# Optimization experiments

Hardware: AMD Instinct MI355X
Metric: run time of the kernel (lower is better)

Reference implementation:

```python
import jax, jax.numpy as jnp
import numpy as np

B, N, T, C, H, HH, ED, HOR, OC = 16, 307, 12, 2, 64, 64, 8, 12, 1


def setup_inputs() -> dict:
    key = jax.random.key(0)
    ks = jax.random.split(key, 23)
    r = lambda i, shape: jax.random.normal(ks[i], shape, dtype=jnp.float32) * 0.1
    return dict(
        coeff_a=r(0, (B, N, T - 1, C)), coeff_b=r(1, (B, N, T - 1, C)),
        coeff_c=r(2, (B, N, T - 1, C)), coeff_d=r(3, (B, N, T - 1, C)),
        times=jnp.arange(T, dtype=jnp.float32),
        h_W=r(4, (C, H)), h_b=r(5, (H,)),
        z_W=r(6, (C, H)), z_b=r(7, (H,)),
        f_W_in=r(8, (H, HH)), f_b_in=r(9, (HH,)),
        f_W_mid=r(10, (HH, HH)), f_b_mid=r(11, (HH,)),
        f_W_out=r(12, (HH, H * C)), f_b_out=r(13, (H * C,)),
        g_W_in=r(14, (H, HH)), g_b_in=r(15, (HH,)),
        g_E=r(16, (N, ED)), g_Wpool=r(17, (ED, 2, HH, HH)), g_bpool=r(18, (ED, HH)),
        g_W_out=r(19, (HH, H * H)), g_b_out=r(20, (H * H,)),
        conv_W=r(21, (HOR * OC, H)), conv_b=r(22, (HOR * OC,)),
    )


def _forward(coeff_a, coeff_b, coeff_c, coeff_d, times,
             h_W, h_b, z_W, z_b,
             f_W_in, f_b_in, f_W_mid, f_b_mid, f_W_out, f_b_out,
             g_W_in, g_b_in, g_E, g_Wpool, g_bpool, g_W_out, g_b_out,
             conv_W, conv_b):
    n_int = times.shape[0] - 1

    def spline_deriv(t):
        # natural cubic spline derivative: b + (two_c + three_d*frac)*frac on interval idx
        idx = jnp.clip(jnp.searchsorted(times, t, side='right') - 1, 0, n_int - 1)
        frac = t - times[idx]
        bb = jnp.take(coeff_b, idx, axis=2)
        cc = jnp.take(coeff_c, idx, axis=2)
        dd = jnp.take(coeff_d, idx, axis=2)
        return bb + (cc + dd * frac) * frac  # (B,N,C)

    def func_f(h):
        x = jax.nn.relu(h @ f_W_in + f_b_in)
        x = jax.nn.relu(x @ f_W_mid + f_b_mid)
        x = (x @ f_W_out + f_b_out).reshape(*x.shape[:-1], H, C)
        return jnp.tanh(x)  # (B,N,H,C)

    # adaptive adjacency (constant across time, depends only on node embeddings)
    A = jax.nn.softmax(jax.nn.relu(g_E @ g_E.T), axis=1)       # (N,N)
    supports = jnp.stack([jnp.eye(N, dtype=A.dtype), A])       # (K=2,N,N)
    agc_W = jnp.einsum('nd,dkio->nkio', g_E, g_Wpool)          # (N,K,HH,HH)
    agc_b = g_E @ g_bpool                                      # (N,HH)

    def func_g(z):
        x = jax.nn.relu(z @ g_W_in + g_b_in)                   # (B,N,HH)
        x_g = jnp.einsum('knm,bmc->bnkc', supports, x)         # (B,N,K,HH)
        x = jnp.einsum('bnki,nkio->bno', x_g, agc_W) + agc_b   # (B,N,HH)
        x = jax.nn.relu(x)
        x = (x @ g_W_out + g_b_out).reshape(*x.shape[:-1], H, H)
        return jnp.tanh(x)  # (B,N,H,H)

    def vf(t, h, z):
        dX = spline_deriv(t)                                   # (B,N,C)
        f_v = func_f(h)                                        # (B,N,H,C)
        g_v = func_g(z)                                        # (B,N,H,H)
        dh = jnp.einsum('bnhc,bnc->bnh', f_v, dX)
        fg = jnp.einsum('bnij,bnjc->bnic', g_v, f_v)           # (B,N,H,C)
        dz = jnp.einsum('bnhc,bnc->bnh', fg, dX)
        return dh, dz

    # initial states from spline value at times[0] (= coeff_a at interval 0, frac 0)
    x0 = coeff_a[:, :, 0, :]                                   # (B,N,C)
    h0 = x0 @ h_W + h_b
    z0 = x0 @ z_W + z_b

    def step(carry, ts):
        h, z = carry
        t0, t1 = ts
        dt = t1 - t0
        k1h, k1z = vf(t0, h, z)
        k2h, k2z = vf(t0 + dt / 2, h + dt / 2 * k1h, z + dt / 2 * k1z)
        k3h, k3z = vf(t0 + dt / 2, h + dt / 2 * k2h, z + dt / 2 * k2z)
        k4h, k4z = vf(t1, h + dt * k3h, z + dt * k3z)
        h = h + dt / 6 * (k1h + 2 * k2h + 2 * k3h + k4h)
        z = z + dt / 6 * (k1z + 2 * k2z + 2 * k3z + k4z)
        return (h, z), None

    (hT, zT), _ = jax.lax.scan(step, (h0, z0), (times[:-1], times[1:]))

    # end_conv: Conv2d(1, HOR*OC, kernel=(1,H)) over (B,1,N,H) == linear over H
    out = jnp.einsum('bnh,oh->bon', zT, conv_W) + conv_b[None, :, None]  # (B,HOR*OC,N)
    out = out.reshape(B, HOR, OC, N).transpose(0, 1, 3, 2)               # (B,HOR,N,OC)
    return out


def reference(coeff_a, coeff_b, coeff_c, coeff_d, times,
              h_W, h_b, z_W, z_b,
              f_W_in, f_b_in, f_W_mid, f_b_mid, f_W_out, f_b_out,
              g_W_in, g_b_in, g_E, g_Wpool, g_bpool, g_W_out, g_b_out,
              conv_W, conv_b):
    return _forward(coeff_a, coeff_b, coeff_c, coeff_d, times,
                    h_W, h_b, z_W, z_b,
                    f_W_in, f_b_in, f_W_mid, f_b_mid, f_W_out, f_b_out,
                    g_W_in, g_b_in, g_E, g_Wpool, g_bpool, g_W_out, g_b_out,
                    conv_W, conv_b)
```

## Files before the change

kernel.cpp:

```cpp
#include <hip/hip_runtime.h>

#define NB 16
#define NN 307
#define NI 11

typedef __attribute__((ext_vector_type(8))) short bf16x8;
typedef __attribute__((ext_vector_type(4))) float f32x4;

#define OFF_ABF    0u
#define OFF_AGCWT  51200u
#define OFF_AGCB   1308672u
#define OFF_WT     1329152u
#define OFF_H      1460224u
#define OFF_Z      1774592u
#define OFF_KZ     2088960u
#define OFF_ACCZ   2403328u
#define OFF_XBF    2717696u
#define OFF_XGBF   2881536u
#define OFF_XT     3045376u
#define OFF_KHALL  3209216u

#define STG_STRIDE 314368u

__device__ __forceinline__ float tanh_fast(float x){
    float e = __expf(2.0f * x);
    return 1.0f - 2.0f * __builtin_amdgcn_rcpf(e + 1.0f);
}
__device__ __forceinline__ unsigned short f2bf(float f){
    unsigned u = __builtin_bit_cast(unsigned, f);
    unsigned r = u + 0x7FFFu + ((u >> 16) & 1u);
    return (unsigned short)(r >> 16);
}


__global__ void kA(const float* __restrict__ gE, unsigned short* __restrict__ Abf){
    int n = blockIdx.x;
    int lane = threadIdx.x;
    if (n >= NN){
#pragma unroll
        for (int ii = 0; ii < 5; ii++) Abf[n*320 + lane + 64*ii] = 0;
        return;
    }
    float en[8];
#pragma unroll
    for (int d = 0; d < 8; d++) en[d] = gE[n*8 + d];
    float vals[5];
    float mx = -1e30f;
#pragma unroll
    for (int ii = 0; ii < 5; ii++){
        int m = lane + 64*ii;
        float v = -1e30f;
        if (m < NN){
            float a = 0.f;
#pragma unroll
            for (int d = 0; d < 8; d++) a += en[d] * gE[m*8 + d];
            v = fmaxf(a, 0.f);
        }
        vals[ii] = v;
        mx = fmaxf(mx, v);
    }
#pragma unroll
    for (int off = 32; off >= 1; off >>= 1) mx = fmaxf(mx, __shfl_xor(mx, off, 64));
    float s = 0.f;
#pragma unroll
    for (int ii = 0; ii < 5; ii++){
        int m = lane + 64*ii;
        if (m < NN){ vals[ii] = __expf(vals[ii] - mx); s += vals[ii]; }
    }
#pragma unroll
    for (int off = 32; off >= 1; off >>= 1) s += __shfl_xor(s, off, 64);
    float inv = 1.f / s;
#pragma unroll
    for (int ii = 0; ii < 5; ii++){
        int m = lane + 64*ii;
        unsigned short v = 0;
        if (m < NN) v = f2bf(vals[ii] * inv);
        Abf[n*320 + m] = v;
    }
}

__global__ __launch_bounds__(256) void kAgcWT(const float* __restrict__ gE,
                                              const float* __restrict__ gWpool,
                                              unsigned short* __restrict__ agcWt){
    __shared__ float t[128*65];
    int tid = threadIdx.x;
    int n = blockIdx.x;
    float ge[8];
#pragma unroll
    for (int d = 0; d < 8; d++) ge[d] = gE[n*8 + d];
    for (int it = 0; it < 32; it++){
        int e = it*256 + tid;
        int o = e & 63, i = (e >> 6) & 63, kk = e >> 12;
        float acc = 0.f;
#pragma unroll
        for (int d = 0; d < 8; d++) acc += ge[d] * gWpool[((size_t)(d*2 + kk)*64 + i)*64 + o];
        t[(kk*64 + i)*65 + o] = acc;
    }
    __syncthreads();
    for (int it = 0; it < 32; it++){
        int e = it*256 + tid;
        int k = e & 127, o = e >> 7;
        agcWt[((size_t)n*64 + o)*128 + k] = f2bf(t[k*65 + o]);
    }
}

__global__ void kAgcB(const float* __restrict__ gE, const float* __restrict__ gbpool,
                      float* __restrict__ agcb){
    int gid = blockIdx.x*256 + threadIdx.x;
    if (gid >= NN*64) return;
    int o = gid & 63;
    int n = gid >> 6;
    float acc = 0.f;
#pragma unroll
    for (int d = 0; d < 8; d++) acc += gE[n*8 + d] * gbpool[d*64 + o];
    agcb[gid] = acc;
}

__global__ __launch_bounds__(256) void kWt(const float* __restrict__ WgOut,
                                           unsigned short* __restrict__ Wt_sw){
    __shared__ float t[64*65];
    int tid = threadIdx.x;
    int c0 = blockIdx.x*64;
    for (int it = 0; it < 16; it++){
        int e = it*256 + tid;
        int k = e >> 6, c = e & 63;
        t[k*65 + c] = WgOut[(size_t)k*4096 + c0 + c];
    }
    __syncthreads();
    for (int it = 0; it < 16; it++){
        int e = it*256 + tid;
        int c = e >> 6, k = e & 63;
        int ks = ((((k >> 3) ^ (c & 7)) << 3) | (k & 7));
        Wt_sw[(size_t)(c0 + c)*64 + ks] = f2bf(t[k*65 + c]);
    }
}

__global__ void kZeroTail(unsigned short* __restrict__ xT){
    int gid = blockIdx.x*256 + threadIdx.x;
    int mo = gid & 15, c = (gid >> 4) & 63, b = gid >> 10;
    xT[((size_t)b*64 + c)*320 + 304 + mo] = 0;
}

__global__ void kInit(const float* __restrict__ ca,
                      const float* __restrict__ hW, const float* __restrict__ hb,
                      const float* __restrict__ zW, const float* __restrict__ zb,
                      float* __restrict__ h, float* __restrict__ z){
    int gid = blockIdx.x*256 + threadIdx.x;
    int t = gid & 63;
    int bn = gid >> 6;
    float x0 = ca[bn*NI*2 + 0];
    float x1 = ca[bn*NI*2 + 1];
    h[gid] = x0*hW[t] + x1*hW[64 + t] + hb[t];
    z[gid] = x0*zW[t] + x1*zW[64 + t] + zb[t];
}

__global__ __launch_bounds__(256) void KH(
    const float* __restrict__ h0, float* __restrict__ khAll,
    const float* __restrict__ Cb, const float* __restrict__ Cc, const float* __restrict__ Cd,
    const float* __restrict__ WfIn, const float* __restrict__ fbIn,
    const float* __restrict__ WfMid, const float* __restrict__ fbMid,
    const float* __restrict__ WfOut, const float* __restrict__ fbOut)
{
    __shared__ float4 bufA[4][16];
    __shared__ float4 bufB[4][16];
    int tid = threadIdx.x;
    int wv = tid >> 6;
    int lane = tid & 63;
    int bn = blockIdx.x*4 + wv;
    int base = bn*64 + lane;

    float hv = h0[base];
    float acch = 0.f, khprev = 0.f;

#pragma unroll 1
    for (int stage = 0; stage < 44; stage++){
        int step = stage >> 2, s = stage & 3;
        float acoef = (s == 0) ? 0.f : (s == 3 ? 1.f : 0.5f);
        int idx; float frac;
        if (s == 0)        { idx = step;     frac = 0.f;  }
        else if (s < 3)    { idx = step;     frac = 0.5f; }
        else if (step < 10){ idx = step + 1; frac = 0.f;  }
        else               { idx = 10;       frac = 1.f;  }

        float sih = hv + acoef * khprev;
        ((float*)&bufA[wv][0])[lane] = sih;

        float a0 = fbIn[lane], a1 = 0.f, a2 = 0.f, a3 = 0.f;
#pragma unroll
        for (int k4 = 0; k4 < 16; k4 += 2){
            float4 s4 = bufA[wv][k4];
            float4 s5 = bufA[wv][k4+1];
            int k = k4*4;
            a0 += s4.x*WfIn[(k+0)*64 + lane];
            a1 += s4.y*WfIn[(k+1)*64 + lane];
            a2 += s4.z*WfIn[(k+2)*64 + lane];
            a3 += s4.w*WfIn[(k+3)*64 + lane];
            a0 += s5.x*WfIn[(k+4)*64 + lane];
            a1 += s5.y*WfIn[(k+5)*64 + lane];
            a2 += s5.z*WfIn[(k+6)*64 + lane];
            a3 += s5.w*WfIn[(k+7)*64 + lane];
        }
        float u = fmaxf((a0 + a1) + (a2 + a3), 0.f);
        ((float*)&bufB[wv][0])[lane] = u;

        float c0_ = fbMid[lane], c1_ = 0.f, c2_ = 0.f, c3_ = 0.f;
#pragma unroll
        for (int k4 = 0; k4 < 16; k4 += 2){
            float4 s4 = bufB[wv][k4];
            float4 s5 = bufB[wv][k4+1];
            int k = k4*4;
            c0_ += s4.x*WfMid[(k+0)*64 + lane];
            c1_ += s4.y*WfMid[(k+1)*64 + lane];
            c2_ += s4.z*WfMid[(k+2)*64 + lane];
            c3_ += s4.w*WfMid[(k+3)*64 + lane];
            c0_ += s5.x*WfMid[(k+4)*64 + lane];
            c1_ += s5.y*WfMid[(k+5)*64 + lane];
            c2_ += s5.z*WfMid[(k+6)*64 + lane];
            c3_ += s5.w*WfMid[(k+7)*64 + lane];
        }
        float u2v = fmaxf((c0_ + c1_) + (c2_ + c3_), 0.f);
        ((float*)&bufA[wv][0])[lane] = u2v;

        float f0a = fbOut[lane*2 + 0], f0b = 0.f;
        float f1a = fbOut[lane*2 + 1], f1b = 0.f;
#pragma unroll
        for (int k4 = 0; k4 < 16; k4 += 2){
            float4 s4 = bufA[wv][k4];
            float4 s5 = bufA[wv][k4+1];
            int k = k4*4;
            f0a += s4.x*WfOut[(k+0)*128 + lane*2+0]; f1a += s4.x*WfOut[(k+0)*128 + lane*2+1];
            f0b += s4.y*WfOut[(k+1)*128 + lane*2+0]; f1b += s4.y*WfOut[(k+1)*128 + lane*2+1];
            f0a += s4.z*WfOut[(k+2)*128 + lane*2+0]; f1a += s4.z*WfOut[(k+2)*128 + lane*2+1];
            f0b += s4.w*WfOut[(k+3)*128 + lane*2+0]; f1b += s4.w*WfOut[(k+3)*128 + lane*2+1];
            f0a += s5.x*WfOut[(k+4)*128 + lane*2+0]; f1a += s5.x*WfOut[(k+4)*128 + lane*2+1];
            f0b += s5.y*WfOut[(k+5)*128 + lane*2+0]; f1b += s5.y*WfOut[(k+5)*128 + lane*2+1];
            f0a += s5.z*WfOut[(k+6)*128 + lane*2+0]; f1a += s5.z*WfOut[(k+6)*128 + lane*2+1];
            f0b += s5.w*WfOut[(k+7)*128 + lane*2+0]; f1b += s5.w*WfOut[(k+7)*128 + lane*2+1];
        }
        float f0 = tanh_fast(f0a + f0b);
        float f1 = tanh_fast(f1a + f1b);

        int cb = (bn*NI + idx)*2;
        float b0 = Cb[cb], b1 = Cb[cb+1];
        float c0 = Cc[cb], c1 = Cc[cb+1];
        float d0 = Cd[cb], d1 = Cd[cb+1];
        float dx0 = b0 + (c0 + d0*frac)*frac;
        float dx1 = b1 + (c1 + d1*frac)*frac;

        float khv = f0*dx0 + f1*dx1;
        khAll[(size_t)stage*STG_STRIDE + base] = khv;
        if (s == 0)      acch = khv;
        else if (s < 3)  acch += 2.f*khv;
        else             hv = hv + (1.f/6.f)*(acch + khv);
        khprev = khv;
    }
}

__global__ __launch_bounds__(256) void Kz1(
    const float* __restrict__ z, const float* __restrict__ kz,
    unsigned short* __restrict__ xbf, unsigned short* __restrict__ xT,
    const float* __restrict__ WgIn, const float* __restrict__ gbIn,
    int stage, float acoef)
{
    __shared__ float4 bufZ[4][16];
    int tid = threadIdx.x;
    int wv = tid >> 6;
    int lane = tid & 63;
    int bn = blockIdx.x*4 + wv;
    int base = bn*64 + lane;
    int b = (int)((unsigned)bn / 307u);
    int n = bn - b*307;

    float siz = z[base];
    if (stage > 0) siz += acoef * kz[base];
    ((float*)&bufZ[wv][0])[lane] = siz;

    float xa = gbIn[lane], xb = 0.f;
#pragma unroll
    for (int k4 = 0; k4 < 16; k4 += 2){
        float4 z4 = bufZ[wv][k4];
        float4 z5 = bufZ[wv][k4+1];
        int k = k4*4;
        xa += z4.x*WgIn[(k+0)*64 + lane];
        xb += z4.y*WgIn[(k+1)*64 + lane];
        xa += z4.z*WgIn[(k+2)*64 + lane];
        xb += z4.w*WgIn[(k+3)*64 + lane];
        xa += z5.x*WgIn[(k+4)*64 + lane];
        xb += z5.y*WgIn[(k+5)*64 + lane];
        xa += z5.z*WgIn[(k+6)*64 + lane];
        xb += z5.w*WgIn[(k+7)*64 + lane];
    }
    unsigned short xbfv = f2bf(fmaxf(xa + xb, 0.f));
    xbf[((size_t)n*16 + b)*64 + lane] = xbfv;
    xT[((size_t)b*64 + lane)*320 + n] = xbfv;
}

__global__ __launch_bounds__(256) void KXG(
    const unsigned short* __restrict__ xT, const unsigned short* __restrict__ Abf,
    unsigned short* __restrict__ xgbf)
{
    int tid = threadIdx.x, lane = tid & 63, wv = tid >> 6;
    int quad = lane >> 4, l15 = lane & 15;
    int b = blockIdx.x / 20, nt = blockIdx.x % 20;
    int n0 = nt*16;

    f32x4 acc = {0.f,0.f,0.f,0.f};
#pragma unroll
    for (int mt = 0; mt < 10; mt++){
        bf16x8 a  = *(const bf16x8*)(Abf + (size_t)(n0 + l15)*320 + mt*32 + quad*8);
        bf16x8 bb = *(const bf16x8*)(xT + ((size_t)b*64 + wv*16 + l15)*320 + mt*32 + quad*8);
        acc = __builtin_amdgcn_mfma_f32_16x16x32_bf16(a, bb, acc, 0, 0, 0);
    }
#pragma unroll
    for (int r = 0; r < 4; r++){
        int n = n0 + quad*4 + r;
        xgbf[((size_t)n*16 + b)*64 + wv*16 + l15] = f2bf(acc[r]);
    }
}

__global__ __launch_bounds__(256, 3) void K2f(
    float* __restrict__ z, const float* __restrict__ khS,
    float* __restrict__ kz, float* __restrict__ accz,
    const unsigned short* __restrict__ xbf, const unsigned short* __restrict__ xgbf,
    const unsigned short* __restrict__ agcWt, const float* __restrict__ agcb,
    const unsigned short* __restrict__ Wt_sw, const float* __restrict__ gbOut,
    int stage)
{
    __shared__ unsigned short WtL[256*64];
    __shared__ unsigned short Ybf[64*68];
    __shared__ float dzl[4*16*5];
    int tid = threadIdx.x, lane = tid & 63, wv = tid >> 6;
    int quad = lane >> 4, l15 = lane & 15;
    int nt = blockIdx.x >> 4, cg = blockIdx.x & 15;
    int n0 = nt*4;
    int nw = n0 + wv;
    int n = nw < NN ? nw : NN-1;
    int C0 = cg*256;

#pragma unroll
    for (int it = 0; it < 8; it++){
        int seg = it*256 + wv*64 + lane;
        const unsigned short* src = Wt_sw + (size_t)C0*64 + (size_t)seg*8;
        __builtin_amdgcn_global_load_lds(
            (const __attribute__((address_space(1))) void*)src,
            (__attribute__((address_space(3))) void*)(WtL + (it*256 + wv*64)*8),
            16, 0, 0);
    }

    float4 khr[4];
#pragma unroll
    for (int c = 0; c < 4; c++)
        khr[c] = *(const float4*)(khS + ((size_t)l15*NN + n)*64 + c*16 + quad*4);

    {
        const size_t xrow = ((size_t)n*16 + l15)*64;
        bf16x8 a[4];
        a[0] = *(const bf16x8*)(xbf  + xrow + 0  + quad*8);
        a[1] = *(const bf16x8*)(xbf  + xrow + 32 + quad*8);
        a[2] = *(const bf16x8*)(xgbf + xrow + 0  + quad*8);
        a[3] = *(const bf16x8*)(xgbf + xrow + 32 + quad*8);
#pragma unroll
        for (int ot = 0; ot < 4; ot++){
            f32x4 acc = {0.f,0.f,0.f,0.f};
#pragma unroll
            for (int kt = 0; kt < 4; kt++){
                bf16x8 bbb = *(const bf16x8*)(agcWt + ((size_t)n*64 + ot*16 + l15)*128 + kt*32 + quad*8);
                acc = __builtin_amdgcn_mfma_f32_16x16x32_bf16(a[kt], bbb, acc, 0, 0, 0);
            }
            float gb = agcb[n*64 + ot*16 + l15];
#pragma unroll
            for (int r = 0; r < 4; r++)
                Ybf[(wv*16 + quad*4 + r)*68 + ot*16 + l15] = f2bf(fmaxf(acc[r] + gb, 0.f));
        }
    }

    __syncthreads();

    bf16x8 bb0 = *(const bf16x8*)(Ybf + (wv*16 + l15)*68 + 0  + quad*8);
    bf16x8 bb1 = *(const bf16x8*)(Ybf + (wv*16 + l15)*68 + 32 + quad*8);

    int sw = l15 & 7;
#pragma unroll
    for (int i4 = 0; i4 < 4; i4++){
        float pacc = 0.f;
#pragma unroll
        for (int c4 = 0; c4 < 4; c4++){
            int ct = i4*4 + c4;
            int row = ct*16 + l15;
            f32x4 acc = {0.f,0.f,0.f,0.f};
            bf16x8 a0 = *(const bf16x8*)(WtL + row*64 + (((quad)     ^ sw) << 3));
            acc = __builtin_amdgcn_mfma_f32_16x16x32_bf16(a0, bb0, acc, 0, 0, 0);
            bf16x8 a1 = *(const bf16x8*)(WtL + row*64 + (((4 + quad) ^ sw) << 3));
            acc = __builtin_amdgcn_mfma_f32_16x16x32_bf16(a1, bb1, acc, 0, 0, 0);
            float4 gb4 = *(const float4*)(gbOut + C0 + ct*16 + quad*4);
            float4 kh4 = khr[c4];
            pacc += tanh_fast(acc[0] + gb4.x) * kh4.x
                  + tanh_fast(acc[1] + gb4.y) * kh4.y
                  + tanh_fast(acc[2] + gb4.z) * kh4.z
                  + tanh_fast(acc[3] + gb4.w) * kh4.w;
        }
        pacc += __shfl_xor(pacc, 16, 64);
        pacc += __shfl_xor(pacc, 32, 64);
        if (quad == 0) dzl[(wv*16 + l15)*5 + i4] = pacc;
    }

    {
        int w = tid >> 6, bb_ = (tid >> 2) & 15, il = tid & 3;
        int nn = n0 + w;
        if (nn < NN){
            size_t addr = ((size_t)bb_*NN + nn)*64 + cg*4 + il;
            float v = dzl[(w*16 + bb_)*5 + il];
            kz[addr] = v;
            if (stage == 0)      accz[addr] = v;
            else if (stage < 3)  accz[addr] += 2.f*v;
            else                 z[addr] += (1.f/6.f)*(accz[addr] + v);
        }
    }
}

__global__ __launch_bounds__(256) void kOut(const float* __restrict__ z,
                                            const float* __restrict__ convW,
                                            const float* __restrict__ convB,
                                            float* __restrict__ out){
    int gid = blockIdx.x*256 + threadIdx.x;
    if (gid >= NB*NN) return;
    int b = gid / NN, n = gid % NN;
    float zr[64];
    const float4* zp = (const float4*)(z + (size_t)gid*64);
#pragma unroll
    for (int k4 = 0; k4 < 16; k4++){
        float4 v = zp[k4];
        zr[k4*4+0] = v.x; zr[k4*4+1] = v.y; zr[k4*4+2] = v.z; zr[k4*4+3] = v.w;
    }
#pragma unroll
    for (int o = 0; o < 12; o++){
        float acc = convB[o];
#pragma unroll
        for (int hh = 0; hh < 64; hh++) acc += zr[hh]*convW[o*64 + hh];
        out[(b*12 + o)*NN + n] = acc;
    }
}

extern "C" void kernel_launch(void* const* d_in, const int* in_sizes, int n_in,
                              void* d_out, int out_size, void* d_ws, size_t ws_size,
                              hipStream_t stream)
{
    const float* coeff_a = (const float*)d_in[0];
    const float* coeff_b = (const float*)d_in[1];
    const float* coeff_c = (const float*)d_in[2];
    const float* coeff_d = (const float*)d_in[3];
    const float* hW     = (const float*)d_in[5];
    const float* hb     = (const float*)d_in[6];
    const float* zW     = (const float*)d_in[7];
    const float* zb     = (const float*)d_in[8];
    const float* WfIn   = (const float*)d_in[9];
    const float* fbIn   = (const float*)d_in[10];
    const float* WfMid  = (const float*)d_in[11];
    const float* fbMid  = (const float*)d_in[12];
    const float* WfOut  = (const float*)d_in[13];
    const float* fbOut  = (const float*)d_in[14];
    const float* WgIn   = (const float*)d_in[15];
    const float* gbIn   = (const float*)d_in[16];
    const float* gE     = (const float*)d_in[17];
    const float* gWpool = (const float*)d_in[18];
    const float* gbpool = (const float*)d_in[19];
    const float* WgOut  = (const float*)d_in[20];
    const float* gbOut  = (const float*)d_in[21];
    const float* convW  = (const float*)d_in[22];
    const float* convB  = (const float*)d_in[23];

    float* ws = (float*)d_ws;
    unsigned short* Abf   = (unsigned short*)(ws + OFF_ABF);
    unsigned short* agcWt = (unsigned short*)(ws + OFF_AGCWT);
    float*          agcb  = ws + OFF_AGCB;
    unsigned short* Wt_sw = (unsigned short*)(ws + OFF_WT);
    float* h     = ws + OFF_H;
    float* z     = ws + OFF_Z;
    float* kz    = ws + OFF_KZ;
    float* accz  = ws + OFF_ACCZ;
    unsigned short* xbf  = (unsigned short*)(ws + OFF_XBF);
    unsigned short* xgbf = (unsigned short*)(ws + OFF_XGBF);
    unsigned short* xT   = (unsigned short*)(ws + OFF_XT);
    float* khAll = ws + OFF_KHALL;
    float* out = (float*)d_out;

    kA        <<<320, 64,  0, stream>>>(gE, Abf);
    kAgcWT    <<<NN,  256, 0, stream>>>(gE, gWpool, agcWt);
    kAgcB     <<<77,  256, 0, stream>>>(gE, gbpool, agcb);
    kWt       <<<64,  256, 0, stream>>>(WgOut, Wt_sw);
    kZeroTail <<<64,  256, 0, stream>>>(xT);
    kInit     <<<1228,256, 0, stream>>>(coeff_a, hW, hb, zW, zb, h, z);

    KH<<<1228, 256, 0, stream>>>(h, khAll, coeff_b, coeff_c, coeff_d,
                                 WfIn, fbIn, WfMid, fbMid, WfOut, fbOut);

    const float acoef[4] = {0.f, 0.5f, 0.5f, 1.f};
    for (int step = 0; step < 11; step++){
        for (int s = 0; s < 4; s++){
            const float* khS = khAll + (size_t)(step*4 + s)*STG_STRIDE;
            Kz1<<<1228, 256, 0, stream>>>(z, kz, xbf, xT, WgIn, gbIn, s, acoef[s]);
            KXG<<<320, 256, 0, stream>>>(xT, Abf, xgbf);
            K2f<<<1232, 256, 0, stream>>>(z, khS, kz, accz, xbf, xgbf,
                                          agcWt, agcb, Wt_sw, gbOut, s);
        }
    }
    kOut<<<20, 256, 0, stream>>>(z, convW, convB, out);
}
```

Measured before the change: 2.094 ms.

## Fuse g input layer into graph aggregation kernel via MFMA; two nodes per wave in KH

Merges the per-stage Kz1 and KXG kernels into one KXZ kernel. It computes relu(z_stage @ WgIn + b) with bf16 MFMA into a shared-memory transposed tile, then runs the adjacency MFMA from LDS, which removes one launch per stage (44 in total) and the global xT round trip. The cost is that each of the 20 node-tile blocks per batch recomputes the full input projection for all 307 nodes, so that work is duplicated 20x. Separately, KH now processes two nodes per wave so each weight load is shared across two rows, halving its grid.

Result: slower. 3.243 ms (+54.9%).

```diff
diff --git a/kernel.cpp b/kernel.cpp
--- a/kernel.cpp
+++ b/kernel.cpp
@@ -5,6 +5,7 @@
 #define NI 11
 
 typedef __attribute__((ext_vector_type(8))) short bf16x8;
+typedef __attribute__((ext_vector_type(4))) short bf16x4;
 typedef __attribute__((ext_vector_type(4))) float f32x4;
 
 #define OFF_ABF    0u
@@ -17,7 +18,7 @@
 #define OFF_ACCZ   2403328u
 #define OFF_XBF    2717696u
 #define OFF_XGBF   2881536u
-#define OFF_XT     3045376u
+#define OFF_WGINT  3045376u
 #define OFF_KHALL  3209216u
 
 #define STG_STRIDE 314368u
@@ -135,10 +136,10 @@
     }
 }
 
-__global__ void kZeroTail(unsigned short* __restrict__ xT){
+__global__ void kWgInT(const float* __restrict__ WgIn, unsigned short* __restrict__ WgInT){
     int gid = blockIdx.x*256 + threadIdx.x;
-    int mo = gid & 15, c = (gid >> 4) & 63, b = gid >> 10;
-    xT[((size_t)b*64 + c)*320 + 304 + mo] = 0;
+    int c = gid >> 6, k = gid & 63;
+    WgInT[gid] = f2bf(WgIn[k*64 + c]);
 }
 
 __global__ void kInit(const float* __restrict__ ca,
@@ -161,16 +162,17 @@
     const float* __restrict__ WfMid, const float* __restrict__ fbMid,
     const float* __restrict__ WfOut, const float* __restrict__ fbOut)
 {
-    __shared__ float4 bufA[4][16];
-    __shared__ float4 bufB[4][16];
+    __shared__ float4 bufA[4][2][16];
+    __shared__ float4 bufB[4][2][16];
     int tid = threadIdx.x;
     int wv = tid >> 6;
     int lane = tid & 63;
-    int bn = blockIdx.x*4 + wv;
-    int base = bn*64 + lane;
-
-    float hv = h0[base];
-    float acch = 0.f, khprev = 0.f;
+    int bn0 = (blockIdx.x*4 + wv)*2;
+    int base0 = bn0*64 + lane;
+
+    float hv0 = h0[base0];
+    float hv1 = h0[base0 + 64];
+    float acch0 = 0.f, khp0 = 0.f, acch1 = 0.f, khp1 = 0.f;
 
 #pragma unroll 1
     for (int stage = 0; stage < 44; stage++){
@@ -182,139 +184,178 @@
         else if (step < 10){ idx = step + 1; frac = 0.f;  }
         else               { idx = 10;       frac = 1.f;  }
 
-        float sih = hv + acoef * khprev;
-        ((float*)&bufA[wv][0])[lane] = sih;
+        ((float*)&bufA[wv][0][0])[lane] = hv0 + acoef*khp0;
+        ((float*)&bufA[wv][1][0])[lane] = hv1 + acoef*khp1;
 
         float a0 = fbIn[lane], a1 = 0.f, a2 = 0.f, a3 = 0.f;
+        float e0 = fbIn[lane], e1 = 0.f, e2 = 0.f, e3 = 0.f;
 #pragma unroll
         for (int k4 = 0; k4 < 16; k4 += 2){
-            float4 s4 = bufA[wv][k4];
-            float4 s5 = bufA[wv][k4+1];
+            float4 s4 = bufA[wv][0][k4];
+            float4 s5 = bufA[wv][0][k4+1];
+            float4 t4 = bufA[wv][1][k4];
+            float4 t5 = bufA[wv][1][k4+1];
             int k = k4*4;
-            a0 += s4.x*WfIn[(k+0)*64 + lane];
-            a1 += s4.y*WfIn[(k+1)*64 + lane];
-            a2 += s4.z*WfIn[(k+2)*64 + lane];
-            a3 += s4.w*WfIn[(k+3)*64 + lane];
-            a0 += s5.x*WfIn[(k+4)*64 + lane];
-            a1 += s5.y*WfIn[(k+5)*64 + lane];
-            a2 += s5.z*WfIn[(k+6)*64 + lane];
-            a3 += s5.w*WfIn[(k+7)*64 + lane];
-        }
-        float u = fmaxf((a0 + a1) + (a2 + a3), 0.f);
-        ((float*)&bufB[wv][0])[lane] = u;
+            float w;
+            w = WfIn[(k+0)*64 + lane]; a0 += s4.x*w; e0 += t4.x*w;
+            w = WfIn[(k+1)*64 + lane]; a1 += s4.y*w; e1 += t4.y*w;
+            w = WfIn[(k+2)*64 + lane]; a2 += s4.z*w; e2 += t4.z*w;
+            w = WfIn[(k+3)*64 + lane]; a3 += s4.w*w; e3 += t4.w*w;
+            w = WfIn[(k+4)*64 + lane]; a0 += s5.x*w; e0 += t5.x*w;
+            w = WfIn[(k+5)*64 + lane]; a1 += s5.y*w; e1 += t5.y*w;
+            w = WfIn[(k+6)*64 + lane]; a2 += s5.z*w; e2 += t5.z*w;
+            w = WfIn[(k+7)*64 + lane]; a3 += s5.w*w; e3 += t5.w*w;
+        }
+        ((float*)&bufB[wv][0][0])[lane] = fmaxf((a0 + a1) + (a2 + a3), 0.f);
+        ((float*)&bufB[wv][1][0])[lane] = fmaxf((e0 + e1) + (e2 + e3), 0.f);
 
         float c0_ = fbMid[lane], c1_ = 0.f, c2_ = 0.f, c3_ = 0.f;
+        float g0_ = fbMid[lane], g1_ = 0.f, g2_ = 0.f, g3_ = 0.f;
 #pragma unroll
         for (int k4 = 0; k4 < 16; k4 += 2){
-            float4 s4 = bufB[wv][k4];
-            float4 s5 = bufB[wv][k4+1];
+            float4 s4 = bufB[wv][0][k4];
+            float4 s5 = bufB[wv][0][k4+1];
+            float4 t4 = bufB[wv][1][k4];
+            float4 t5 = bufB[wv][1][k4+1];
             int k = k4*4;
-            c0_ += s4.x*WfMid[(k+0)*64 + lane];
-            c1_ += s4.y*WfMid[(k+1)*64 + lane];
-            c2_ += s4.z*WfMid[(k+2)*64 + lane];
-            c3_ += s4.w*WfMid[(k+3)*64 + lane];
-            c0_ += s5.x*WfMid[(k+4)*64 + lane];
-            c1_ += s5.y*WfMid[(k+5)*64 + lane];
-            c2_ += s5.z*WfMid[(k+6)*64 + lane];
-            c3_ += s5.w*WfMid[(k+7)*64 + lane];
-        }
-        float u2v = fmaxf((c0_ + c1_) + (c2_ + c3_), 0.f);
-        ((float*)&bufA[wv][0])[lane] = u2v;
-
-        float f0a = fbOut[lane*2 + 0], f0b = 0.f;
-        float f1a = fbOut[lane*2 + 1], f1b = 0.f;
+            float w;
+            w = WfMid[(k+0)*64 + lane]; c0_ += s4.x*w; g0_ += t4.x*w;
+            w = WfMid[(k+1)*64 + lane]; c1_ += s4.y*w; g1_ += t4.y*w;
+            w = WfMid[(k+2)*64 + lane]; c2_ += s4.z*w; g2_ += t4.z*w;
+            w = WfMid[(k+3)*64 + lane]; c3_ += s4.w*w; g3_ += t4.w*w;
+            w = WfMid[(k+4)*64 + lane]; c0_ += s5.x*w; g0_ += t5.x*w;
+            w = WfMid[(k+5)*64 + lane]; c1_ += s5.y*w; g1_ += t5.y*w;
+            w = WfMid[(k+6)*64 + lane]; c2_ += s5.z*w; g2_ += t5.z*w;
+            w = WfMid[(k+7)*64 + lane]; c3_ += s5.w*w; g3_ += t5.w*w;
+        }
+        ((float*)&bufA[wv][0][0])[lane] = fmaxf((c0_ + c1_) + (c2_ + c3_), 0.f);
+        ((float*)&bufA[wv][1][0])[lane] = fmaxf((g0_ + g1_) + (g2_ + g3_), 0.f);
+
+        float p0a = fbOut[lane*2 + 0], p0b = 0.f;
+        float p1a = fbOut[lane*2 + 1], p1b = 0.f;
+        float q0a = fbOut[lane*2 + 0], q0b = 0.f;
+        float q1a = fbOut[lane*2 + 1], q1b = 0.f;
 #pragma unroll
         for (int k4 = 0; k4 < 16; k4 += 2){
-            float4 s4 = bufA[wv][k4];
-            float4 s5 = bufA[wv][k4+1];
+            float4 s4 = bufA[wv][0][k4];
+            float4 s5 = bufA[wv][0][k4+1];
+            float4 t4 = bufA[wv][1][k4];
+            float4 t5 = bufA[wv][1][k4+1];
             int k = k4*4;
-            f0a += s4.x*WfOut[(k+0)*128 + lane*2+0]; f1a += s4.x*WfOut[(k+0)*128 + lane*2+1];
-            f0b += s4.y*WfOut[(k+1)*128 + lane*2+0]; f1b += s4.y*WfOut[(k+1)*128 + lane*2+1];
-            f0a += s4.z*WfOut[(k+2)*128 + lane*2+0]; f1a += s4.z*WfOut[(k+2)*128 + lane*2+1];
-            f0b += s4.w*WfOut[(k+3)*128 + lane*2+0]; f1b += s4.w*WfOut[(k+3)*128 + lane*2+1];
-            f0a += s5.x*WfOut[(k+4)*128 + lane*2+0]; f1a += s5.x*WfOut[(k+4)*128 + lane*2+1];
-            f0b += s5.y*WfOut[(k+5)*128 + lane*2+0]; f1b += s5.y*WfOut[(k+5)*128 + lane*2+1];
-            f0a += s5.z*WfOut[(k+6)*128 + lane*2+0]; f1a += s5.z*WfOut[(k+6)*128 + lane*2+1];
-            f0b += s5.w*WfOut[(k+7)*128 + lane*2+0]; f1b += s5.w*WfOut[(k+7)*128 + lane*2+1];
-        }
-        float f0 = tanh_fast(f0a + f0b);
-        float f1 = tanh_fast(f1a + f1b);
-
-        int cb = (bn*NI + idx)*2;
-        float b0 = Cb[cb], b1 = Cb[cb+1];
-        float c0 = Cc[cb], c1 = Cc[cb+1];
-        float d0 = Cd[cb], d1 = Cd[cb+1];
-        float dx0 = b0 + (c0 + d0*frac)*frac;
-        float dx1 = b1 + (c1 + d1*frac)*frac;
-
-        float khv = f0*dx0 + f1*dx1;
-        khAll[(size_t)stage*STG_STRIDE + base] = khv;
-        if (s == 0)      acch = khv;
-        else if (s < 3)  acch += 2.f*khv;
-        else             hv = hv + (1.f/6.f)*(acch + khv);
-        khprev = khv;
-    }
-}
-
-__global__ __launch_bounds__(256) void Kz1(
+            float w0, w1;
+            w0 = WfOut[(k+0)*128 + lane*2+0]; w1 = WfOut[(k+0)*128 + lane*2+1];
+            p0a += s4.x*w0; p1a += s4.x*w1; q0a += t4.x*w0; q1a += t4.x*w1;
+            w0 = WfOut[(k+1)*128 + lane*2+0]; w1 = WfOut[(k+1)*128 + lane*2+1];
+            p0b += s4.y*w0; p1b += s4.y*w1; q0b += t4.y*w0; q1b += t4.y*w1;
+            w0 = WfOut[(k+2)*128 + lane*2+0]; w1 = WfOut[(k+2)*128 + lane*2+1];
+            p0a += s4.z*w0; p1a += s4.z*w1; q0a += t4.z*w0; q1a += t4.z*w1;
+            w0 = WfOut[(k+3)*128 + lane*2+0]; w1 = WfOut[(k+3)*128 + lane*2+1];
+            p0b += s4.w*w0; p1b += s4.w*w1; q0b += t4.w*w0; q1b += t4.w*w1;
+            w0 = WfOut[(k+4)*128 + lane*2+0]; w1 = WfOut[(k+4)*128 + lane*2+1];
+            p0a += s5.x*w0; p1a += s5.x*w1; q0a += t5.x*w0; q1a += t5.x*w1;
+            w0 = WfOut[(k+5)*128 + lane*2+0]; w1 = WfOut[(k+5)*128 + lane*2+1];
+            p0b += s5.y*w0; p1b += s5.y*w1; q0b += t5.y*w0; q1b += t5.y*w1;
+            w0 = WfOut[(k+6)*128 + lane*2+0]; w1 = WfOut[(k+6)*128 + lane*2+1];
+            p0a += s5.z*w0; p1a += s5.z*w1; q0a += t5.z*w0; q1a += t5.z*w1;
+            w0 = WfOut[(k+7)*128 + lane*2+0]; w1 = WfOut[(k+7)*128 + lane*2+1];
+            p0b += s5.w*w0; p1b += s5.w*w1; q0b += t5.w*w0; q1b += t5.w*w1;
+        }
+        float f00 = tanh_fast(p0a + p0b);
+        float f01 = tanh_fast(p1a + p1b);
+        float f10 = tanh_fast(q0a + q0b);
+        float f11 = tanh_fast(q1a + q1b);
+
+        int cb0 = (bn0*NI + idx)*2;
+        int cb1 = cb0 + NI*2;
+        float dx00 = Cb[cb0]   + (Cc[cb0]   + Cd[cb0]*frac)*frac;
+        float dx01 = Cb[cb0+1] + (Cc[cb0+1] + Cd[cb0+1]*frac)*frac;
+        float dx10 = Cb[cb1]   + (Cc[cb1]   + Cd[cb1]*frac)*frac;
+        float dx11 = Cb[cb1+1] + (Cc[cb1+1] + Cd[cb1+1]*frac)*frac;
+
+        float kh0 = f00*dx00 + f01*dx01;
+        float kh1 = f10*dx10 + f11*dx11;
+        khAll[(size_t)stage*STG_STRIDE + base0]      = kh0;
+        khAll[(size_t)stage*STG_STRIDE + base0 + 64] = kh1;
+        if (s == 0)     { acch0 = kh0;        acch1 = kh1; }
+        else if (s < 3) { acch0 += 2.f*kh0;   acch1 += 2.f*kh1; }
+        else            { hv0 += (1.f/6.f)*(acch0 + kh0); hv1 += (1.f/6.f)*(acch1 + kh1); }
+        khp0 = kh0; khp1 = kh1;
+    }
+}
+
+__global__ __launch_bounds__(256) void KXZ(
     const float* __restrict__ z, const float* __restrict__ kz,
-    unsigned short* __restrict__ xbf, unsigned short* __restrict__ xT,
-    const float* __restrict__ WgIn, const float* __restrict__ gbIn,
+    const unsigned short* __restrict__ WgInT, const float* __restrict__ gbIn,
+    const unsigned short* __restrict__ Abf,
+    unsigned short* __restrict__ xbf, unsigned short* __restrict__ xgbf,
     int stage, float acoef)
 {
-    __shared__ float4 bufZ[4][16];
-    int tid = threadIdx.x;
-    int wv = tid >> 6;
-    int lane = tid & 63;
-    int bn = blockIdx.x*4 + wv;
-    int base = bn*64 + lane;
-    int b = (int)((unsigned)bn / 307u);
-    int n = bn - b*307;
-
-    float siz = z[base];
-    if (stage > 0) siz += acoef * kz[base];
-    ((float*)&bufZ[wv][0])[lane] = siz;
-
-    float xa = gbIn[lane], xb = 0.f;
-#pragma unroll
-    for (int k4 = 0; k4 < 16; k4 += 2){
-        float4 z4 = bufZ[wv][k4];
-        float4 z5 = bufZ[wv][k4+1];
-        int k = k4*4;
-        xa += z4.x*WgIn[(k+0)*64 + lane];
-        xb += z4.y*WgIn[(k+1)*64 + lane];
-        xa += z4.z*WgIn[(k+2)*64 + lane];
-        xb += z4.w*WgIn[(k+3)*64 + lane];
-        xa += z5.x*WgIn[(k+4)*64 + lane];
-        xb += z5.y*WgIn[(k+5)*64 + lane];
-        xa += z5.z*WgIn[(k+6)*64 + lane];
-        xb += z5.w*WgIn[(k+7)*64 + lane];
-    }
-    unsigned short xbfv = f2bf(fmaxf(xa + xb, 0.f));
-    xbf[((size_t)n*16 + b)*64 + lane] = xbfv;
-    xT[((size_t)b*64 + lane)*320 + n] = xbfv;
-}
-
-__global__ __launch_bounds__(256) void KXG(
-    const unsigned short* __restrict__ xT, const unsigned short* __restrict__ Abf,
-    unsigned short* __restrict__ xgbf)
-{
+    __shared__ unsigned short xLT[64*328];
     int tid = threadIdx.x, lane = tid & 63, wv = tid >> 6;
     int quad = lane >> 4, l15 = lane & 15;
     int b = blockIdx.x / 20, nt = blockIdx.x % 20;
     int n0 = nt*16;
+    int cc = wv*16 + l15;
+
+    bf16x8 wb0 = *(const bf16x8*)(WgInT + cc*64 + quad*8);
+    bf16x8 wb1 = *(const bf16x8*)(WgInT + cc*64 + 32 + quad*8);
+    float gb = gbIn[cc];
+    bool writer = (nt == 0);
+
+#pragma unroll 1
+    for (int mt = 0; mt < 20; mt++){
+        int m = mt*16 + l15;
+        bf16x8 af0 = {0,0,0,0,0,0,0,0};
+        bf16x8 af1 = {0,0,0,0,0,0,0,0};
+        if (m < NN){
+            const float* zp = z + ((size_t)b*NN + m)*64;
+            float4 x0 = *(const float4*)(zp + quad*8);
+            float4 x1 = *(const float4*)(zp + quad*8 + 4);
+            float4 y0 = *(const float4*)(zp + 32 + quad*8);
+            float4 y1 = *(const float4*)(zp + 32 + quad*8 + 4);
+            if (stage > 0){
+                const float* kp = kz + ((size_t)b*NN + m)*64;
+                float4 k0 = *(const float4*)(kp + quad*8);
+                float4 k1 = *(const float4*)(kp + quad*8 + 4);
+                float4 k2 = *(const float4*)(kp + 32 + quad*8);
+                float4 k3 = *(const float4*)(kp + 32 + quad*8 + 4);
+                x0.x += acoef*k0.x; x0.y += acoef*k0.y; x0.z += acoef*k0.z; x0.w += acoef*k0.w;
+                x1.x += acoef*k1.x; x1.y += acoef*k1.y; x1.z += acoef*k1.z; x1.w += acoef*k1.w;
+                y0.x += acoef*k2.x; y0.y += acoef*k2.y; y0.z += acoef*k2.z; y0.w += acoef*k2.w;
+                y1.x += acoef*k3.x; y1.y += acoef*k3.y; y1.z += acoef*k3.z; y1.w += acoef*k3.w;
+            }
+            unsigned short* p0 = (unsigned short*)&af0;
+            unsigned short* p1 = (unsigned short*)&af1;
+            p0[0]=f2bf(x0.x); p0[1]=f2bf(x0.y); p0[2]=f2bf(x0.z); p0[3]=f2bf(x0.w);
+            p0[4]=f2bf(x1.x); p0[5]=f2bf(x1.y); p0[6]=f2bf(x1.z); p0[7]=f2bf(x1.w);
+            p1[0]=f2bf(y0.x); p1[1]=f2bf(y0.y); p1[2]=f2bf(y0.z); p1[3]=f2bf(y0.w);
+            p1[4]=f2bf(y1.x); p1[5]=f2bf(y1.y); p1[6]=f2bf(y1.z); p1[7]=f2bf(y1.w);
+        }
+        f32x4 acc = {0.f,0.f,0.f,0.f};
+        acc = __builtin_amdgcn_mfma_f32_16x16x32_bf16(af0, wb0, acc, 0, 0, 0);
+        acc = __builtin_amdgcn_mfma_f32_16x16x32_bf16(af1, wb1, acc, 0, 0, 0);
+        bf16x4 pk;
+#pragma unroll
+        for (int r = 0; r < 4; r++){
+            int mm = mt*16 + quad*4 + r;
+            unsigned short v = f2bf(fmaxf(acc[r] + gb, 0.f));
+            ((unsigned short*)&pk)[r] = v;
+            if (writer && mm < NN) xbf[((size_t)mm*16 + b)*64 + cc] = v;
+        }
+        *(bf16x4*)(xLT + cc*328 + mt*16 + quad*4) = pk;
+    }
 
     f32x4 acc = {0.f,0.f,0.f,0.f};
 #pragma unroll
-    for (int mt = 0; mt < 10; mt++){
-        bf16x8 a  = *(const bf16x8*)(Abf + (size_t)(n0 + l15)*320 + mt*32 + quad*8);
-        bf16x8 bb = *(const bf16x8*)(xT + ((size_t)b*64 + wv*16 + l15)*320 + mt*32 + quad*8);
+    for (int mt2 = 0; mt2 < 10; mt2++){
+        bf16x8 a  = *(const bf16x8*)(Abf + (size_t)(n0 + l15)*320 + mt2*32 + quad*8);
+        bf16x8 bb = *(const bf16x8*)(xLT + cc*328 + mt2*32 + quad*8);
         acc = __builtin_amdgcn_mfma_f32_16x16x32_bf16(a, bb, acc, 0, 0, 0);
     }
 #pragma unroll
     for (int r = 0; r < 4; r++){
         int n = n0 + quad*4 + r;
-        xgbf[((size_t)n*16 + b)*64 + wv*16 + l15] = f2bf(acc[r]);
+        xgbf[((size_t)n*16 + b)*64 + cc] = f2bf(acc[r]);
     }
 }
 
@@ -478,28 +519,28 @@
     float* z     = ws + OFF_Z;
     float* kz    = ws + OFF_KZ;
     float* accz  = ws + OFF_ACCZ;
-    unsigned short* xbf  = (unsigned short*)(ws + OFF_XBF);
-    unsigned short* xgbf = (unsigned short*)(ws + OFF_XGBF);
-    unsigned short* xT   = (unsigned short*)(ws + OFF_XT);
+    unsigned short* xbf   = (unsigned short*)(ws + OFF_XBF);
+    unsigned short* xgbf  = (unsigned short*)(ws + OFF_XGBF);
+    unsigned short* WgInT = (unsigned short*)(ws + OFF_WGINT);
     float* khAll = ws + OFF_KHALL;
     float* out = (float*)d_out;
 
-    kA        <<<320, 64,  0, stream>>>(gE, Abf);
-    kAgcWT    <<<NN,  256, 0, stream>>>(gE, gWpool, agcWt);
-    kAgcB     <<<77,  256, 0, stream>>>(gE, gbpool, agcb);
-    kWt       <<<64,  256, 0, stream>>>(WgOut, Wt_sw);
-    kZeroTail <<<64,  256, 0, stream>>>(xT);
-    kInit     <<<1228,256, 0, stream>>>(coeff_a, hW, hb, zW, zb, h, z);
-
-    KH<<<1228, 256, 0, stream>>>(h, khAll, coeff_b, coeff_c, coeff_d,
-                                 WfIn, fbIn, WfMid, fbMid, WfOut, fbOut);
+    kA     <<<320, 64,  0, stream>>>(gE, Abf);
+    kAgcWT <<<NN,  256, 0, stream>>>(gE, gWpool, agcWt);
+    kAgcB  <<<77,  256, 0, stream>>>(gE, gbpool, agcb);
+    kWt    <<<64,  256, 0, stream>>>(WgOut, Wt_sw);
+    kWgInT <<<16,  256, 0, stream>>>(WgIn, WgInT);
+    kInit  <<<1228,256, 0, stream>>>(coeff_a, hW, hb, zW, zb, h, z);
+
+    KH<<<614, 256, 0, stream>>>(h, khAll, coeff_b, coeff_c, coeff_d,
+                                WfIn, fbIn, WfMid, fbMid, WfOut, fbOut);
 
     const float acoef[4] = {0.f, 0.5f, 0.5f, 1.f};
     for (int step = 0; step < 11; step++){
         for (int s = 0; s < 4; s++){
             const float* khS = khAll + (size_t)(step*4 + s)*STG_STRIDE;
-            Kz1<<<1228, 256, 0, stream>>>(z, kz, xbf, xT, WgIn, gbIn, s, acoef[s]);
-            KXG<<<320, 256, 0, stream>>>(xT, Abf, xgbf);
+            KXZ<<<320, 256, 0, stream>>>(z, kz, WgInT, gbIn, Abf,
+                                         xbf, xgbf, s, acoef[s]);
             K2f<<<1232, 256, 0, stream>>>(z, khS, kz, accz, xbf, xgbf,
                                           agcWt, agcb, Wt_sw, gbOut, s);
         }
```
